# Kernel optimization log

Measured on AMD Instinct MI355X. Metric: run time of the kernel, lower is better.

The kernel has to match this reference:

```python
import jax, jax.numpy as jnp
import numpy as np

N, E, IN, H, OUT, K = 50000, 800000, 128, 128, 40, 10
ALPHA, EPS, AH = 0.1, 1e-5, 64


def setup_inputs() -> dict:
    key = jax.random.key(0)
    ks = jax.random.split(key, 32)
    rn = lambda k, s, sc=0.05: jax.random.normal(k, s, jnp.float32) * sc
    return dict(
        x=jax.random.normal(ks[0], (N, IN), jnp.float32),
        edge_index=jax.random.randint(ks[1], (2, E), 0, N, jnp.int64),
        edge_weight=jax.random.uniform(ks[2], (E,), jnp.float32),
        lin1_w=rn(ks[3], (H, IN)), lin1_b=rn(ks[4], (H,)),
        bn1_g=jnp.ones((H,), jnp.float32), bn1_b=jnp.zeros((H,), jnp.float32),
        bn1_m=rn(ks[5], (H,)), bn1_v=jax.random.uniform(ks[6], (H,), jnp.float32, 0.5, 1.5),
        lin2_w=rn(ks[7], (H, H)), lin2_b=rn(ks[8], (H,)),
        bn2_g=jnp.ones((H,), jnp.float32), bn2_b=jnp.zeros((H,), jnp.float32),
        bn2_m=rn(ks[9], (H,)), bn2_v=jax.random.uniform(ks[10], (H,), jnp.float32, 0.5, 1.5),
        att1_w=rn(ks[11], (AH, 2 * H)), att1_b=rn(ks[12], (AH,)),
        att2_w=rn(ks[13], (K + 1, AH)), att2_b=rn(ks[14], (K + 1,)),
        head1_w=rn(ks[15], (H // 2, H)), head1_b=rn(ks[16], (H // 2,)),
        bn3_g=jnp.ones((H // 2,), jnp.float32), bn3_b=jnp.zeros((H // 2,), jnp.float32),
        bn3_m=rn(ks[17], (H // 2,)), bn3_v=jax.random.uniform(ks[18], (H // 2,), jnp.float32, 0.5, 1.5),
        head2_w=rn(ks[19], (OUT, H // 2)), head2_b=rn(ks[20], (OUT,)),
    )


def _bn(x, g, b, m, v):
    # eval-mode BatchNorm1d with running stats
    return (x - m) * jax.lax.rsqrt(v + EPS) * g + b


def reference(x, edge_index, edge_weight,
              lin1_w, lin1_b, bn1_g, bn1_b, bn1_m, bn1_v,
              lin2_w, lin2_b, bn2_g, bn2_b, bn2_m, bn2_v,
              att1_w, att1_b, att2_w, att2_b,
              head1_w, head1_b, bn3_g, bn3_b, bn3_m, bn3_v,
              head2_w, head2_b):
    row, col = edge_index[0], edge_index[1]

    # dense stem (dropout is identity in eval mode)
    h = jax.nn.relu(_bn(x @ lin1_w.T + lin1_b, bn1_g, bn1_b, bn1_m, bn1_v))
    identity = h
    h = jax.nn.relu(_bn(h @ lin2_w.T + lin2_b, bn2_g, bn2_b, bn2_m, bn2_v)) + identity
    base = h  # h0 for APPNP

    # edge normalization (loop-invariant): w_e / clamp(sum_w(row), 1)
    wsum = jnp.clip(jax.ops.segment_sum(edge_weight, row, num_segments=N), 1.0)
    enorm = edge_weight / wsum[row]  # [E]

    xs = [h]
    for _ in range(K):  # fixed K iterations of gather -> scatter-add
        agg = jax.ops.segment_sum(h[row] * enorm[:, None], col, num_segments=N)
        h = (1.0 - ALPHA) * agg + ALPHA * base
        xs.append(h)

    stacked = jnp.stack(xs, axis=-1)                    # [N, H, K+1]
    ctx = jnp.concatenate([xs[0], xs[-1]], axis=-1)     # [N, 2H]
    a = jax.nn.gelu(ctx @ att1_w.T + att1_b, approximate=False) @ att2_w.T + att2_b
    w = jax.nn.softmax(a, axis=-1)[:, None, :]          # [N, 1, K+1]
    fused = (stacked * w).sum(axis=-1)                  # [N, H]

    z = jax.nn.relu(_bn(fused @ head1_w.T + head1_b, bn3_g, bn3_b, bn3_m, bn3_v))
    return z @ head2_w.T + head2_b
```

## Files before the change

### kernel.cpp

```cpp
#include <hip/hip_runtime.h>
#include <hip/hip_fp16.h>
#include <math.h>

#define NN 50000
#define EE 800000
#define HH 128
#define KIT 10
#define NHF (NN * HH)

typedef _Float16 half8 __attribute__((ext_vector_type(8)));
typedef float floatx4 __attribute__((ext_vector_type(4)));

__device__ __forceinline__ float gelu_exact(float x) {
  return 0.5f * x * (1.f + erff(x * 0.70710678118654752f));
}

__device__ __forceinline__ float4 ld4(const float* p) { return *(const float4*)p; }
__device__ __forceinline__ float4 ld4(const __half* p) {
  const __half2* q = (const __half2*)p;
  float2 lo = __half22float2(q[0]);
  float2 hi = __half22float2(q[1]);
  return make_float4(lo.x, lo.y, hi.x, hi.y);
}
__device__ __forceinline__ void st1(float* p, float v) { *p = v; }
__device__ __forceinline__ void st1(__half* p, float v) { *p = __float2half_rn(v); }

__global__ __launch_bounds__(256) void zero_kernel(float* __restrict__ wsum,
                                                   int* __restrict__ deg, int n) {
  int i = blockIdx.x * 256 + threadIdx.x;
  if (i < n) { wsum[i] = 0.f; deg[i] = 0; }
}

__global__ __launch_bounds__(256) void edge_stats_kernel(const int* __restrict__ ei,
                                                         const float* __restrict__ ew,
                                                         float* __restrict__ wsum,
                                                         int* __restrict__ deg,
                                                         int* __restrict__ rank, int e_cnt) {
  int e = blockIdx.x * 256 + threadIdx.x;
  if (e >= e_cnt) return;
  atomicAdd(&wsum[ei[e]], ew[e]);
  rank[e] = atomicAdd(&deg[ei[EE + e]], 1);
}

__global__ __launch_bounds__(256) void scan1_kernel(const int* __restrict__ deg,
                                                    int* __restrict__ bsum, int n) {
  __shared__ int red[256];
  int i = blockIdx.x * 256 + threadIdx.x;
  red[threadIdx.x] = (i < n) ? deg[i] : 0;
  __syncthreads();
  for (int off = 128; off > 0; off >>= 1) {
    if (threadIdx.x < off) red[threadIdx.x] += red[threadIdx.x + off];
    __syncthreads();
  }
  if (threadIdx.x == 0) bsum[blockIdx.x] = red[0];
}

__global__ __launch_bounds__(256) void scan2_kernel(const int* __restrict__ bsum,
                                                    int* __restrict__ boff,
                                                    int* __restrict__ row_start, int nb, int n) {
  __shared__ int buf[256];
  int tid = threadIdx.x;
  int v = (tid < nb) ? bsum[tid] : 0;
  buf[tid] = v;
  __syncthreads();
  for (int off = 1; off < 256; off <<= 1) {
    int t = (tid >= off) ? buf[tid - off] : 0;
    __syncthreads();
    buf[tid] += t;
    __syncthreads();
  }
  if (tid < nb) boff[tid] = buf[tid] - v;
  if (tid == 255) row_start[n] = buf[255];
}

__global__ __launch_bounds__(256) void scan3_kernel(const int* __restrict__ deg,
                                                    const int* __restrict__ boff,
                                                    int* __restrict__ row_start, int n) {
  __shared__ int buf[256];
  int tid = threadIdx.x;
  int i = blockIdx.x * 256 + tid;
  int v = (i < n) ? deg[i] : 0;
  buf[tid] = v;
  __syncthreads();
  for (int off = 1; off < 256; off <<= 1) {
    int t = (tid >= off) ? buf[tid - off] : 0;
    __syncthreads();
    buf[tid] += t;
    __syncthreads();
  }
  if (i < n) row_start[i] = boff[blockIdx.x] + buf[tid] - v;
}

__global__ __launch_bounds__(256) void csr_fill_kernel(const int* __restrict__ ei,
                                                       const float* __restrict__ ew,
                                                       const float* __restrict__ wsum,
                                                       const int* __restrict__ row_start,
                                                       const int* __restrict__ rank,
                                                       int2* __restrict__ csr, int e_cnt) {
  int e = blockIdx.x * 256 + threadIdx.x;
  if (e >= e_cnt) return;
  int r = ei[e], c = ei[EE + e];
  float ws = wsum[r];
  ws = ws < 1.f ? 1.f : ws;
  float v = 0.9f * ew[e] / ws;
  int pos = row_start[c] + rank[e];
  csr[pos] = make_int2(r, __float_as_int(v));
}

__global__ __launch_bounds__(256) void prop_kernel(const __half* __restrict__ h_cur,
                                                   const __half* __restrict__ base,
                                                   const int* __restrict__ row_start,
                                                   const long* __restrict__ csr,
                                                   __half* __restrict__ h_next) {
  int node = __builtin_amdgcn_readfirstlane((int)blockIdx.x * 4 + (int)(threadIdx.x >> 6));
  if (node >= NN) return;
  int lane = threadIdx.x & 63;
  const __half2* hc = (const __half2*)h_cur;
  float2 b = __half22float2(((const __half2*)base)[(size_t)node * 64 + lane]);
  float ax = 0.1f * b.x, ay = 0.1f * b.y;
  float bx = 0.f, by = 0.f;
  int s = row_start[node], e = row_start[node + 1];
  int i = s;
  for (; i + 8 <= e; i += 8) {
    long c[8];
#pragma unroll
    for (int j = 0; j < 8; ++j) c[j] = csr[i + j];
    float2 g[8];
#pragma unroll
    for (int j = 0; j < 8; ++j) g[j] = __half22float2(hc[(size_t)(int)c[j] * 64 + lane]);
#pragma unroll
    for (int j = 0; j < 8; ++j) {
      float v = __int_as_float((int)(c[j] >> 32));
      if (j & 1) { bx = fmaf(v, g[j].x, bx); by = fmaf(v, g[j].y, by); }
      else       { ax = fmaf(v, g[j].x, ax); ay = fmaf(v, g[j].y, ay); }
    }
  }
  for (; i + 4 <= e; i += 4) {
    long c[4];
#pragma unroll
    for (int j = 0; j < 4; ++j) c[j] = csr[i + j];
    float2 g[4];
#pragma unroll
    for (int j = 0; j < 4; ++j) g[j] = __half22float2(hc[(size_t)(int)c[j] * 64 + lane]);
#pragma unroll
    for (int j = 0; j < 4; ++j) {
      float v = __int_as_float((int)(c[j] >> 32));
      if (j & 1) { bx = fmaf(v, g[j].x, bx); by = fmaf(v, g[j].y, by); }
      else       { ax = fmaf(v, g[j].x, ax); ay = fmaf(v, g[j].y, ay); }
    }
  }
  for (; i < e; ++i) {
    long c0 = csr[i];
    float2 g0 = __half22float2(hc[(size_t)(int)c0 * 64 + lane]);
    float v = __int_as_float((int)(c0 >> 32));
    ax = fmaf(v, g0.x, ax); ay = fmaf(v, g0.y, ay);
  }
  ((__half2*)h_next)[(size_t)node * 64 + lane] =
      __float22half2_rn(make_float2(ax + bx, ay + by));
}

template <int K, int KA, int JP, int JR, int ACT, bool RESID, typename IT, typename OT>
__global__ __launch_bounds__(256) void mfma_dense(
    const IT* __restrict__ Xa, const IT* __restrict__ Xb,
    const float* __restrict__ W, const float* __restrict__ lb,
    const float* __restrict__ bg, const float* __restrict__ bb,
    const float* __restrict__ bm, const float* __restrict__ bv,
    const OT* __restrict__ resid, OT* __restrict__ out) {
  constexpr int KC = (K > 128) ? 128 : K;
  static_assert(K % KC == 0 && KC % 32 == 0 && JP % 16 == 0, "");
  constexpr int JT = JP / 16;
  __shared__ _Float16 xL[128][KC + 8];
  __shared__ _Float16 wL[JP][KC + 8];
  const int tid = threadIdx.x;
  const int wv = tid >> 6, lane = tid & 63;
  const int q = lane >> 4, m = lane & 15;
  const int r0 = blockIdx.x * 128;

  floatx4 acc[2][JT];
#pragma unroll
  for (int rt = 0; rt < 2; ++rt)
#pragma unroll
    for (int jt = 0; jt < JT; ++jt) acc[rt][jt] = (floatx4)(0.f);

  for (int kc = 0; kc < K; kc += KC) {
    __syncthreads();
    for (int idx = tid; idx < 128 * (KC / 4); idx += 256) {
      int r = idx / (KC / 4);
      int c4 = (idx % (KC / 4)) * 4;
      int row = r0 + r;
      int col = kc + c4;
      float4 v = make_float4(0.f, 0.f, 0.f, 0.f);
      if (row < NN) {
        if (col < KA) v = ld4(&Xa[(size_t)row * KA + col]);
        else          v = ld4(&Xb[(size_t)row * (K - KA) + (col - KA)]);
      }
      xL[r][c4 + 0] = (_Float16)v.x; xL[r][c4 + 1] = (_Float16)v.y;
      xL[r][c4 + 2] = (_Float16)v.z; xL[r][c4 + 3] = (_Float16)v.w;
    }
    for (int idx = tid; idx < JP * (KC / 4); idx += 256) {
      int j = idx / (KC / 4);
      int c4 = (idx % (KC / 4)) * 4;
      float4 v = make_float4(0.f, 0.f, 0.f, 0.f);
      if (j < JR) v = *(const float4*)&W[(size_t)j * K + kc + c4];
      wL[j][c4 + 0] = (_Float16)v.x; wL[j][c4 + 1] = (_Float16)v.y;
      wL[j][c4 + 2] = (_Float16)v.z; wL[j][c4 + 3] = (_Float16)v.w;
    }
    __syncthreads();
#pragma unroll
    for (int ks = 0; ks < KC; ks += 32) {
      half8 a0 = *(const half8*)&xL[wv * 32 + m][ks + q * 8];
      half8 a1 = *(const half8*)&xL[wv * 32 + 16 + m][ks + q * 8];
#pragma unroll
      for (int jt = 0; jt < JT; ++jt) {
        half8 b = *(const half8*)&wL[jt * 16 + m][ks + q * 8];
        acc[0][jt] = __builtin_amdgcn_mfma_f32_16x16x32_f16(a0, b, acc[0][jt], 0, 0, 0);
        acc[1][jt] = __builtin_amdgcn_mfma_f32_16x16x32_f16(a1, b, acc[1][jt], 0, 0, 0);
      }
    }
  }
#pragma unroll
  for (int jt = 0; jt < JT; ++jt) {
    int j = jt * 16 + m;
    if (j >= JR) continue;
    float sc = 0.f, sh = 0.f;
    if (ACT == 1) {
      sc = bg[j] * rsqrtf(bv[j] + 1e-5f);
      sh = (lb[j] - bm[j]) * sc + bb[j];
    } else {
      sh = lb[j];
    }
#pragma unroll
    for (int rt = 0; rt < 2; ++rt) {
#pragma unroll
      for (int reg = 0; reg < 4; ++reg) {
        int row = r0 + wv * 32 + rt * 16 + q * 4 + reg;
        if (row >= NN) continue;
        float a = acc[rt][jt][reg];
        float y;
        if (ACT == 0)      y = a + sh;
        else if (ACT == 1) y = fmaxf(fmaf(a, sc, sh), 0.f);
        else               y = gelu_exact(a + sh);
        if (RESID) {
          float4 rv;
          (void)rv;
          y += (float)resid[(size_t)row * JR + j];
        }
        st1(&out[(size_t)row * JR + j], y);
      }
    }
  }
}

__global__ __launch_bounds__(64) void att2_softmax_kernel(const __half* __restrict__ g,
                                                          const float* __restrict__ W2,
                                                          const float* __restrict__ b2,
                                                          float* __restrict__ attw, int n_rows) {
  __shared__ float gl[64][65];
  int r0 = blockIdx.x * 64;
  for (int idx = threadIdx.x; idx < 64 * 16; idx += 64) {
    int r = idx >> 4, c4 = (idx & 15) * 4;
    float4 v = make_float4(0.f, 0.f, 0.f, 0.f);
    if (r0 + r < n_rows) v = ld4(&g[(size_t)(r0 + r) * 64 + c4]);
    gl[r][c4] = v.x; gl[r][c4 + 1] = v.y; gl[r][c4 + 2] = v.z; gl[r][c4 + 3] = v.w;
  }
  __syncthreads();
  int r = threadIdx.x;
  int n = r0 + r;
  if (n >= n_rows) return;
  float a[KIT + 1];
#pragma unroll
  for (int j = 0; j < KIT + 1; ++j) {
    float acc = b2[j];
#pragma unroll
    for (int k = 0; k < 64; ++k) acc = fmaf(gl[r][k], W2[j * 64 + k], acc);
    a[j] = acc;
  }
  float mx = a[0];
#pragma unroll
  for (int j = 1; j < KIT + 1; ++j) mx = fmaxf(mx, a[j]);
  float s = 0.f;
#pragma unroll
  for (int j = 0; j < KIT + 1; ++j) { a[j] = expf(a[j] - mx); s += a[j]; }
  float inv = 1.f / s;
#pragma unroll
  for (int j = 0; j < KIT + 1; ++j) attw[n * 16 + j] = a[j] * inv;
}

__global__ __launch_bounds__(256) void fused_gather_kernel(const __half* __restrict__ XS,
                                                           const float* __restrict__ attw,
                                                           __half* __restrict__ fused) {
  int node = __builtin_amdgcn_readfirstlane((int)blockIdx.x * 4 + (int)(threadIdx.x >> 6));
  if (node >= NN) return;
  int lane = threadIdx.x & 63;
  float ax = 0.f, ay = 0.f;
#pragma unroll
  for (int k = 0; k <= KIT; ++k) {
    float wk = attw[node * 16 + k];
    float2 v = __half22float2(((const __half2*)(XS + (size_t)k * NHF))[(size_t)node * 64 + lane]);
    ax = fmaf(wk, v.x, ax);
    ay = fmaf(wk, v.y, ay);
  }
  ((__half2*)fused)[(size_t)node * 64 + lane] = __float22half2_rn(make_float2(ax, ay));
}

__global__ __launch_bounds__(256) void fused_accum_kernel(const __half* __restrict__ h,
                                                          const float* __restrict__ attw,
                                                          float* __restrict__ fused, int k) {
  int node = __builtin_amdgcn_readfirstlane((int)blockIdx.x * 4 + (int)(threadIdx.x >> 6));
  if (node >= NN) return;
  int lane = threadIdx.x & 63;
  float wk = attw[node * 16 + k];
  float2 v = __half22float2(((const __half2*)h)[(size_t)node * 64 + lane]);
  float2 o;
  if (k == 0) {
    o = make_float2(wk * v.x, wk * v.y);
  } else {
    float2 f = ((const float2*)fused)[(size_t)node * 64 + lane];
    o = make_float2(fmaf(wk, v.x, f.x), fmaf(wk, v.y, f.y));
  }
  ((float2*)fused)[(size_t)node * 64 + lane] = o;
}

extern "C" void kernel_launch(void* const* d_in, const int* in_sizes, int n_in,
                              void* d_out, int out_size, void* d_ws, size_t ws_size,
                              hipStream_t stream) {
  (void)in_sizes; (void)n_in; (void)out_size;
  const float* x      = (const float*)d_in[0];
  const int*   ei     = (const int*)d_in[1];
  const float* ew     = (const float*)d_in[2];
  const float* lin1_w = (const float*)d_in[3];
  const float* lin1_b = (const float*)d_in[4];
  const float* bn1_g  = (const float*)d_in[5];
  const float* bn1_b  = (const float*)d_in[6];
  const float* bn1_m  = (const float*)d_in[7];
  const float* bn1_v  = (const float*)d_in[8];
  const float* lin2_w = (const float*)d_in[9];
  const float* lin2_b = (const float*)d_in[10];
  const float* bn2_g  = (const float*)d_in[11];
  const float* bn2_b  = (const float*)d_in[12];
  const float* bn2_m  = (const float*)d_in[13];
  const float* bn2_v  = (const float*)d_in[14];
  const float* att1_w = (const float*)d_in[15];
  const float* att1_b = (const float*)d_in[16];
  const float* att2_w = (const float*)d_in[17];
  const float* att2_b = (const float*)d_in[18];
  const float* head1_w= (const float*)d_in[19];
  const float* head1_b= (const float*)d_in[20];
  const float* bn3_g  = (const float*)d_in[21];
  const float* bn3_b  = (const float*)d_in[22];
  const float* bn3_m  = (const float*)d_in[23];
  const float* bn3_v  = (const float*)d_in[24];
  const float* head2_w= (const float*)d_in[25];
  const float* head2_b= (const float*)d_in[26];
  float* out = (float*)d_out;

  char* p = (char*)d_ws;
  auto alloc = [&](size_t bytes) -> void* {
    void* r = (void*)p;
    p += (bytes + 255) & ~(size_t)255;
    return r;
  };
  float* wsum     = (float*)alloc((size_t)NN * 4);
  int*   deg      = (int*)alloc((size_t)NN * 4);
  int*   row_start= (int*)alloc((size_t)(NN + 1) * 4);
  int*   rank     = (int*)alloc((size_t)EE * 4);
  int*   bsum     = (int*)alloc((size_t)256 * 4);
  int*   boff     = (int*)alloc((size_t)256 * 4);
  long*  csr      = (long*)alloc((size_t)EE * 8);
  __half* gbuf    = (__half*)alloc((size_t)NN * 64 * 2);
  float* attw     = (float*)alloc((size_t)NN * 16 * 4);
  __half* h1      = (__half*)alloc((size_t)NHF * 2);
  __half* fusedH  = (__half*)alloc((size_t)NHF * 2);
  __half* zbuf    = (__half*)alloc((size_t)NN * 64 * 2);
  size_t common = (size_t)(p - (char*)d_ws);
  size_t stored_need = common + (size_t)(KIT + 1) * NHF * 2 + 4096;
  bool stored = ws_size >= stored_need;

  const int GE = (EE + 255) / 256;
  const int GN = (NN + 255) / 256;
  const int GM = (NN + 127) / 128;
  const int GP = (NN + 3) / 4;
  const int GA = (NN + 63) / 64;

  zero_kernel<<<GN, 256, 0, stream>>>(wsum, deg, NN);
  edge_stats_kernel<<<GE, 256, 0, stream>>>(ei, ew, wsum, deg, rank, EE);
  scan1_kernel<<<GN, 256, 0, stream>>>(deg, bsum, NN);
  scan2_kernel<<<1, 256, 0, stream>>>(bsum, boff, row_start, GN, NN);
  scan3_kernel<<<GN, 256, 0, stream>>>(deg, boff, row_start, NN);
  csr_fill_kernel<<<GE, 256, 0, stream>>>(ei, ew, wsum, row_start, rank, (int2*)csr, EE);

  if (stored) {
    __half* XS = (__half*)alloc((size_t)(KIT + 1) * NHF * 2);
    mfma_dense<128, 128, 128, 128, 1, false, float, __half><<<GM, 256, 0, stream>>>(
        x, (const float*)nullptr, lin1_w, lin1_b, bn1_g, bn1_b, bn1_m, bn1_v, nullptr, h1);
    mfma_dense<128, 128, 128, 128, 1, true, __half, __half><<<GM, 256, 0, stream>>>(
        h1, (const __half*)nullptr, lin2_w, lin2_b, bn2_g, bn2_b, bn2_m, bn2_v, h1, XS);
    for (int k = 0; k < KIT; ++k) {
      prop_kernel<<<GP, 256, 0, stream>>>(XS + (size_t)k * NHF, XS, row_start,
                                          csr, XS + (size_t)(k + 1) * NHF);
    }
    mfma_dense<256, 128, 64, 64, 2, false, __half, __half><<<GM, 256, 0, stream>>>(
        XS, XS + (size_t)KIT * NHF, att1_w, att1_b, nullptr, nullptr, nullptr, nullptr,
        nullptr, gbuf);
    att2_softmax_kernel<<<GA, 64, 0, stream>>>(gbuf, att2_w, att2_b, attw, NN);
    fused_gather_kernel<<<GP, 256, 0, stream>>>(XS, attw, fusedH);
    mfma_dense<128, 128, 64, 64, 1, false, __half, __half><<<GM, 256, 0, stream>>>(
        fusedH, (const __half*)nullptr, head1_w, head1_b, bn3_g, bn3_b, bn3_m, bn3_v,
        nullptr, zbuf);
  } else {
    float*  fusedF = (float*)alloc((size_t)NHF * 4);
    __half* base   = (__half*)alloc((size_t)NHF * 2);
    __half* hA     = (__half*)alloc((size_t)NHF * 2);
    __half* hB     = (__half*)alloc((size_t)NHF * 2);
    mfma_dense<128, 128, 128, 128, 1, false, float, __half><<<GM, 256, 0, stream>>>(
        x, (const float*)nullptr, lin1_w, lin1_b, bn1_g, bn1_b, bn1_m, bn1_v, nullptr, h1);
    mfma_dense<128, 128, 128, 128, 1, true, __half, __half><<<GM, 256, 0, stream>>>(
        h1, (const __half*)nullptr, lin2_w, lin2_b, bn2_g, bn2_b, bn2_m, bn2_v, h1, base);
    const __half* cur = base;
    for (int k = 1; k <= KIT; ++k) {
      __half* nxt = (k & 1) ? hA : hB;
      prop_kernel<<<GP, 256, 0, stream>>>(cur, base, row_start, csr, nxt);
      cur = nxt;
    }
    mfma_dense<256, 128, 64, 64, 2, false, __half, __half><<<GM, 256, 0, stream>>>(
        base, cur, att1_w, att1_b, nullptr, nullptr, nullptr, nullptr, nullptr, gbuf);
    att2_softmax_kernel<<<GA, 64, 0, stream>>>(gbuf, att2_w, att2_b, attw, NN);
    fused_accum_kernel<<<GP, 256, 0, stream>>>(base, attw, fusedF, 0);
    cur = base;
    for (int k = 1; k <= KIT; ++k) {
      __half* nxt = (k & 1) ? hA : hB;
      prop_kernel<<<GP, 256, 0, stream>>>(cur, base, row_start, csr, nxt);
      fused_accum_kernel<<<GP, 256, 0, stream>>>(nxt, attw, fusedF, k);
      cur = nxt;
    }
    mfma_dense<128, 128, 64, 64, 1, false, float, __half><<<GM, 256, 0, stream>>>(
        fusedF, (const float*)nullptr, head1_w, head1_b, bn3_g, bn3_b, bn3_m, bn3_v,
        nullptr, zbuf);
  }

  mfma_dense<64, 64, 48, 40, 0, false, __half, float><<<GM, 256, 0, stream>>>(
      zbuf, (const __half*)nullptr, head2_w, head2_b, nullptr, nullptr, nullptr, nullptr,
      nullptr, out);
}
```

Baseline: 636.9 us.

## Pad atomic counters to stride 16, overlay scratch on XS, prefetch CSR in propagation

The per-node weight-sum and degree counters are spaced 16 words apart so that atomics from different nodes stop contending on shared cache lines. When the stored path is taken, these padded buffers and the rank array are placed in the last XS slice, which is not written until the final propagation step, so no extra workspace is used. The propagation kernel now software-prefetches the next group of 8 CSR entries while it gathers and accumulates the current group, and the 4-wide remainder loop is removed, leaving the 1-wide loop to handle up to 7 leftover edges. The padding increases the zeroing work and makes the scan reads strided.

Measured after the change: 660.6 us. 1.04x slower.

```diff
diff --git a/kernel.cpp b/kernel.cpp
--- a/kernel.cpp
+++ b/kernel.cpp
@@ -7,6 +7,7 @@
 #define HH 128
 #define KIT 10
 #define NHF (NN * HH)
+#define PST 16
 
 typedef _Float16 half8 __attribute__((ext_vector_type(8)));
 typedef float floatx4 __attribute__((ext_vector_type(4)));
@@ -25,28 +26,28 @@
 __device__ __forceinline__ void st1(float* p, float v) { *p = v; }
 __device__ __forceinline__ void st1(__half* p, float v) { *p = __float2half_rn(v); }
 
-__global__ __launch_bounds__(256) void zero_kernel(float* __restrict__ wsum,
-                                                   int* __restrict__ deg, int n) {
+__global__ __launch_bounds__(256) void zero_kernel(float* __restrict__ wsum_p,
+                                                   int* __restrict__ deg_p, int n) {
   int i = blockIdx.x * 256 + threadIdx.x;
-  if (i < n) { wsum[i] = 0.f; deg[i] = 0; }
+  if (i < n) { wsum_p[i] = 0.f; deg_p[i] = 0; }
 }
 
 __global__ __launch_bounds__(256) void edge_stats_kernel(const int* __restrict__ ei,
                                                          const float* __restrict__ ew,
-                                                         float* __restrict__ wsum,
-                                                         int* __restrict__ deg,
+                                                         float* __restrict__ wsum_p,
+                                                         int* __restrict__ deg_p,
                                                          int* __restrict__ rank, int e_cnt) {
   int e = blockIdx.x * 256 + threadIdx.x;
   if (e >= e_cnt) return;
-  atomicAdd(&wsum[ei[e]], ew[e]);
-  rank[e] = atomicAdd(&deg[ei[EE + e]], 1);
-}
-
-__global__ __launch_bounds__(256) void scan1_kernel(const int* __restrict__ deg,
+  atomicAdd(&wsum_p[(size_t)ei[e] * PST], ew[e]);
+  rank[e] = atomicAdd(&deg_p[(size_t)ei[EE + e] * PST], 1);
+}
+
+__global__ __launch_bounds__(256) void scan1_kernel(const int* __restrict__ deg_p,
                                                     int* __restrict__ bsum, int n) {
   __shared__ int red[256];
   int i = blockIdx.x * 256 + threadIdx.x;
-  red[threadIdx.x] = (i < n) ? deg[i] : 0;
+  red[threadIdx.x] = (i < n) ? deg_p[(size_t)i * PST] : 0;
   __syncthreads();
   for (int off = 128; off > 0; off >>= 1) {
     if (threadIdx.x < off) red[threadIdx.x] += red[threadIdx.x + off];
@@ -73,13 +74,13 @@
   if (tid == 255) row_start[n] = buf[255];
 }
 
-__global__ __launch_bounds__(256) void scan3_kernel(const int* __restrict__ deg,
+__global__ __launch_bounds__(256) void scan3_kernel(const int* __restrict__ deg_p,
                                                     const int* __restrict__ boff,
                                                     int* __restrict__ row_start, int n) {
   __shared__ int buf[256];
   int tid = threadIdx.x;
   int i = blockIdx.x * 256 + tid;
-  int v = (i < n) ? deg[i] : 0;
+  int v = (i < n) ? deg_p[(size_t)i * PST] : 0;
   buf[tid] = v;
   __syncthreads();
   for (int off = 1; off < 256; off <<= 1) {
@@ -93,14 +94,14 @@
 
 __global__ __launch_bounds__(256) void csr_fill_kernel(const int* __restrict__ ei,
                                                        const float* __restrict__ ew,
-                                                       const float* __restrict__ wsum,
+                                                       const float* __restrict__ wsum_p,
                                                        const int* __restrict__ row_start,
                                                        const int* __restrict__ rank,
                                                        int2* __restrict__ csr, int e_cnt) {
   int e = blockIdx.x * 256 + threadIdx.x;
   if (e >= e_cnt) return;
   int r = ei[e], c = ei[EE + e];
-  float ws = wsum[r];
+  float ws = wsum_p[(size_t)r * PST];
   ws = ws < 1.f ? 1.f : ws;
   float v = 0.9f * ew[e] / ws;
   int pos = row_start[c] + rank[e];
@@ -120,31 +121,36 @@
   float ax = 0.1f * b.x, ay = 0.1f * b.y;
   float bx = 0.f, by = 0.f;
   int s = row_start[node], e = row_start[node + 1];
+  int nfull = (e - s) >> 3;
   int i = s;
-  for (; i + 8 <= e; i += 8) {
-    long c[8];
-#pragma unroll
-    for (int j = 0; j < 8; ++j) c[j] = csr[i + j];
+  if (nfull > 0) {
+    long cur[8];
+#pragma unroll
+    for (int j = 0; j < 8; ++j) cur[j] = csr[i + j];
+    i += 8;
+    for (int bidx = 1; bidx < nfull; ++bidx) {
+      long nxt[8];
+#pragma unroll
+      for (int j = 0; j < 8; ++j) nxt[j] = csr[i + j];
+      i += 8;
+      float2 g[8];
+#pragma unroll
+      for (int j = 0; j < 8; ++j) g[j] = __half22float2(hc[(size_t)(int)cur[j] * 64 + lane]);
+#pragma unroll
+      for (int j = 0; j < 8; ++j) {
+        float v = __int_as_float((int)(cur[j] >> 32));
+        if (j & 1) { bx = fmaf(v, g[j].x, bx); by = fmaf(v, g[j].y, by); }
+        else       { ax = fmaf(v, g[j].x, ax); ay = fmaf(v, g[j].y, ay); }
+      }
+#pragma unroll
+      for (int j = 0; j < 8; ++j) cur[j] = nxt[j];
+    }
     float2 g[8];
 #pragma unroll
-    for (int j = 0; j < 8; ++j) g[j] = __half22float2(hc[(size_t)(int)c[j] * 64 + lane]);
+    for (int j = 0; j < 8; ++j) g[j] = __half22float2(hc[(size_t)(int)cur[j] * 64 + lane]);
 #pragma unroll
     for (int j = 0; j < 8; ++j) {
-      float v = __int_as_float((int)(c[j] >> 32));
-      if (j & 1) { bx = fmaf(v, g[j].x, bx); by = fmaf(v, g[j].y, by); }
-      else       { ax = fmaf(v, g[j].x, ax); ay = fmaf(v, g[j].y, ay); }
-    }
-  }
-  for (; i + 4 <= e; i += 4) {
-    long c[4];
-#pragma unroll
-    for (int j = 0; j < 4; ++j) c[j] = csr[i + j];
-    float2 g[4];
-#pragma unroll
-    for (int j = 0; j < 4; ++j) g[j] = __half22float2(hc[(size_t)(int)c[j] * 64 + lane]);
-#pragma unroll
-    for (int j = 0; j < 4; ++j) {
-      float v = __int_as_float((int)(c[j] >> 32));
+      float v = __int_as_float((int)(cur[j] >> 32));
       if (j & 1) { bx = fmaf(v, g[j].x, bx); by = fmaf(v, g[j].y, by); }
       else       { ax = fmaf(v, g[j].x, ax); ay = fmaf(v, g[j].y, ay); }
     }
@@ -240,11 +246,7 @@
         if (ACT == 0)      y = a + sh;
         else if (ACT == 1) y = fmaxf(fmaf(a, sc, sh), 0.f);
         else               y = gelu_exact(a + sh);
-        if (RESID) {
-          float4 rv;
-          (void)rv;
-          y += (float)resid[(size_t)row * JR + j];
-        }
+        if (RESID) y += (float)resid[(size_t)row * JR + j];
         st1(&out[(size_t)row * JR + j], y);
       }
     }
@@ -360,10 +362,7 @@
     p += (bytes + 255) & ~(size_t)255;
     return r;
   };
-  float* wsum     = (float*)alloc((size_t)NN * 4);
-  int*   deg      = (int*)alloc((size_t)NN * 4);
   int*   row_start= (int*)alloc((size_t)(NN + 1) * 4);
-  int*   rank     = (int*)alloc((size_t)EE * 4);
   int*   bsum     = (int*)alloc((size_t)256 * 4);
   int*   boff     = (int*)alloc((size_t)256 * 4);
   long*  csr      = (long*)alloc((size_t)EE * 8);
@@ -376,21 +375,35 @@
   size_t stored_need = common + (size_t)(KIT + 1) * NHF * 2 + 4096;
   bool stored = ws_size >= stored_need;
 
-  const int GE = (EE + 255) / 256;
-  const int GN = (NN + 255) / 256;
-  const int GM = (NN + 127) / 128;
-  const int GP = (NN + 3) / 4;
-  const int GA = (NN + 63) / 64;
-
-  zero_kernel<<<GN, 256, 0, stream>>>(wsum, deg, NN);
-  edge_stats_kernel<<<GE, 256, 0, stream>>>(ei, ew, wsum, deg, rank, EE);
-  scan1_kernel<<<GN, 256, 0, stream>>>(deg, bsum, NN);
+  __half* XS = nullptr;
+  float* wsum_p; int* deg_p; int* rank;
+  if (stored) {
+    XS = (__half*)alloc((size_t)(KIT + 1) * NHF * 2);
+    char* ovl = (char*)(XS + (size_t)KIT * NHF);
+    wsum_p = (float*)ovl;
+    deg_p  = (int*)(ovl + (size_t)NN * PST * 4);
+    rank   = (int*)(ovl + 2 * (size_t)NN * PST * 4);
+  } else {
+    wsum_p = (float*)alloc((size_t)NN * PST * 4);
+    deg_p  = (int*)alloc((size_t)NN * PST * 4);
+    rank   = (int*)alloc((size_t)EE * 4);
+  }
+
+  const int GE  = (EE + 255) / 256;
+  const int GN  = (NN + 255) / 256;
+  const int GN0 = (NN * PST + 255) / 256;
+  const int GM  = (NN + 127) / 128;
+  const int GP  = (NN + 3) / 4;
+  const int GA  = (NN + 63) / 64;
+
+  zero_kernel<<<GN0, 256, 0, stream>>>(wsum_p, deg_p, NN * PST);
+  edge_stats_kernel<<<GE, 256, 0, stream>>>(ei, ew, wsum_p, deg_p, rank, EE);
+  scan1_kernel<<<GN, 256, 0, stream>>>(deg_p, bsum, NN);
   scan2_kernel<<<1, 256, 0, stream>>>(bsum, boff, row_start, GN, NN);
-  scan3_kernel<<<GN, 256, 0, stream>>>(deg, boff, row_start, NN);
-  csr_fill_kernel<<<GE, 256, 0, stream>>>(ei, ew, wsum, row_start, rank, (int2*)csr, EE);
+  scan3_kernel<<<GN, 256, 0, stream>>>(deg_p, boff, row_start, NN);
+  csr_fill_kernel<<<GE, 256, 0, stream>>>(ei, ew, wsum_p, row_start, rank, (int2*)csr, EE);
 
   if (stored) {
-    __half* XS = (__half*)alloc((size_t)(KIT + 1) * NHF * 2);
     mfma_dense<128, 128, 128, 128, 1, false, float, __half><<<GM, 256, 0, stream>>>(
         x, (const float*)nullptr, lin1_w, lin1_b, bn1_g, bn1_b, bn1_m, bn1_v, nullptr, h1);
     mfma_dense<128, 128, 128, 128, 1, true, __half, __half><<<GM, 256, 0, stream>>>(
```
